# Performance work log

Hardware: AMD Instinct MI355X
Metric: run time of the kernel (lower is better)

Reference implementation:

```python
import jax, jax.numpy as jnp
import numpy as np

D_MODEL = 1024
N_HEADS = 16
D_HEAD = 64


def setup_inputs() -> dict:
    key = jax.random.key(0)
    ks = jax.random.split(key, 9)
    B, T = 2, 2048
    s_in = 1.0 / np.sqrt(D_MODEL)
    s_o = 1.0 / np.sqrt(N_HEADS * D_HEAD)
    return {
        "x": jax.random.normal(ks[0], (B, T, D_MODEL), dtype=jnp.float32),
        "wq": jax.random.normal(ks[1], (D_MODEL, N_HEADS * D_HEAD), dtype=jnp.float32) * s_in,
        "bq": jax.random.normal(ks[2], (N_HEADS * D_HEAD,), dtype=jnp.float32) * 0.01,
        "wk": jax.random.normal(ks[3], (D_MODEL, N_HEADS * D_HEAD), dtype=jnp.float32) * s_in,
        "bk": jax.random.normal(ks[4], (N_HEADS * D_HEAD,), dtype=jnp.float32) * 0.01,
        "wv": jax.random.normal(ks[5], (D_MODEL, N_HEADS * D_HEAD), dtype=jnp.float32) * s_in,
        "bv": jax.random.normal(ks[6], (N_HEADS * D_HEAD,), dtype=jnp.float32) * 0.01,
        "wo": jax.random.normal(ks[7], (N_HEADS * D_HEAD, D_MODEL), dtype=jnp.float32) * s_o,
        "bo": jax.random.normal(ks[8], (D_MODEL,), dtype=jnp.float32) * 0.01,
    }


def reference(x, wq, bq, wk, bk, wv, bv, wo, bo):
    B, T, _ = x.shape
    H, Dh = N_HEADS, D_HEAD
    # projections -> [B, H, T, Dh]
    q = (x @ wq + bq).reshape(B, T, H, Dh).transpose(0, 2, 1, 3)
    k = (x @ wk + bk).reshape(B, T, H, Dh).transpose(0, 2, 1, 3)
    v = (x @ wv + bv).reshape(B, T, H, Dh).transpose(0, 2, 1, 3)
    scale = 1.0 / np.sqrt(Dh).astype(np.float32)
    attn = jnp.einsum("bhqd,bhkd->bhqk", q, k) * scale  # [B,H,T,T]
    causal = jnp.tril(jnp.ones((T, T), dtype=bool))
    attn = jnp.where(causal, attn, jnp.float32(-jnp.inf))
    attn = jax.nn.softmax(attn, axis=-1)
    out = jnp.einsum("bhqk,bhkd->bhqd", attn, v)  # [B,H,T,Dh]
    out = out.transpose(0, 2, 1, 3).reshape(B, T, H * Dh)
    return out @ wo + bo
```

## Files before the change

kernel.cpp:

```cpp
#include <hip/hip_runtime.h>
#include <math.h>

#define D_MODEL 1024
#define N_HEADS 16
#define D_HEAD  64
#define B_SZ    2
#define T_SEQ   2048

typedef short bf16x8 __attribute__((ext_vector_type(8)));
typedef short bf16x4 __attribute__((ext_vector_type(4)));
typedef float f32x4  __attribute__((ext_vector_type(4)));
typedef unsigned short us4 __attribute__((ext_vector_type(4)));

__device__ __forceinline__ unsigned short f2bf(float f) {
  union { float f; unsigned u; } v; v.f = f;
  unsigned r = v.u + 0x7FFFu + ((v.u >> 16) & 1u);
  return (unsigned short)(r >> 16);
}
__device__ __forceinline__ float bf2f(unsigned short s) {
  union { unsigned u; float f; } v; v.u = ((unsigned)s) << 16;
  return v.f;
}
__device__ __forceinline__ unsigned pack2_rtz(float lo, float hi) {
  union { float f; unsigned u; } a, b; a.f = hi; b.f = lo;
  return __builtin_amdgcn_perm(a.u, b.u, 0x07060302u);
}

__device__ __forceinline__ void async_copy16(const unsigned short* g, unsigned short* l) {
  __builtin_amdgcn_global_load_lds(
      (__attribute__((address_space(1))) void*)(g),
      (__attribute__((address_space(3))) void*)(l), 16, 0, 0);
}

__global__ __launch_bounds__(256) void conv_all(
    const float* __restrict__ x,
    const float* __restrict__ wq, const float* __restrict__ wk,
    const float* __restrict__ wv, const float* __restrict__ wo,
    unsigned short* __restrict__ wt, unsigned short* __restrict__ xb)
{
  const int z = blockIdx.z;
  if (z < 4) {
    const float* W = (z == 0) ? wq : (z == 1) ? wk : (z == 2) ? wv : wo;
    unsigned short* O = wt + (size_t)z * D_MODEL * D_MODEL;
    __shared__ float t[32][33];
    const int tx = threadIdx.x & 31, ty = threadIdx.x >> 5;
    const int kb = blockIdx.x * 32, nb = blockIdx.y * 32;
    #pragma unroll
    for (int i = 0; i < 4; i++)
      t[ty + i * 8][tx] = W[(size_t)(kb + ty + i * 8) * D_MODEL + nb + tx];
    __syncthreads();
    #pragma unroll
    for (int i = 0; i < 4; i++)
      O[(size_t)(nb + ty + i * 8) * D_MODEL + kb + tx] = f2bf(t[tx][ty + i * 8]);
  } else {
    const int row = (z - 4) * 1024 + blockIdx.y * 32 + (threadIdx.x >> 3);
    const int col = blockIdx.x * 32 + (threadIdx.x & 7) * 4;
    float4 v = *(const float4*)&x[(size_t)row * D_MODEL + col];
    us4 o = { f2bf(v.x), f2bf(v.y), f2bf(v.z), f2bf(v.w) };
    *(us4*)&xb[(size_t)row * D_MODEL + col] = o;
  }
}

#define BKg 64
#define QSCALE 0.180336879f

__global__ __launch_bounds__(256) void qkv_gemm(
    const unsigned short* __restrict__ A, const unsigned short* __restrict__ Bt,
    const float* __restrict__ bq, const float* __restrict__ bk,
    const float* __restrict__ bv, unsigned short* __restrict__ qkv,
    unsigned short* __restrict__ vT)
{
  __shared__ unsigned short As[128 * BKg];
  __shared__ unsigned short Bs[64 * BKg];

  const int tid  = threadIdx.x;
  const int wv   = tid >> 6;
  const int lane = tid & 63;
  const int lr   = lane & 15;
  const int quad = lane >> 4;
  const int wm   = wv >> 1;
  const int wn   = wv & 1;
  const int row0 = blockIdx.x * 128;
  const int col0 = blockIdx.y * 64;
  const int K = D_MODEL;

  const int mid = col0 >> 10;
  const float* bias = (mid == 0) ? bq : (mid == 1) ? bk : bv;

  f32x4 acc[8];
  #pragma unroll
  for (int i = 0; i < 8; i++) acc[i] = (f32x4){0.f, 0.f, 0.f, 0.f};

  for (int k0 = 0; k0 < K; k0 += BKg) {
    #pragma unroll
    for (int it = 0; it < 4; it++) {
      const int gg = wv * 256 + it * 64 + lane;
      const int r  = gg >> 3;
      const int gc = ((gg & 7) ^ (r & 7)) * 8;
      async_copy16(A + (size_t)(row0 + r) * K + k0 + gc,
                   (unsigned short*)As + (size_t)(wv * 256 + it * 64) * 8);
    }
    #pragma unroll
    for (int it = 0; it < 2; it++) {
      const int gg = wv * 128 + it * 64 + lane;
      const int r  = gg >> 3;
      const int gc = ((gg & 7) ^ (r & 7)) * 8;
      async_copy16(Bt + (size_t)(col0 + r) * K + k0 + gc,
                   (unsigned short*)Bs + (size_t)(wv * 128 + it * 64) * 8);
    }
    __syncthreads();

    if (mid == 2) {
      bf16x8 aF[4][2], bF[2][2];
      #pragma unroll
      for (int hf = 0; hf < 2; hf++) {
        const int kc = (hf * 4 + quad) ^ (lr & 7);
        #pragma unroll
        for (int mi = 0; mi < 4; mi++)
          aF[mi][hf] = *(const bf16x8*)&As[(wm * 64 + mi * 16 + lr) * BKg + kc * 8];
        #pragma unroll
        for (int ni = 0; ni < 2; ni++)
          bF[ni][hf] = *(const bf16x8*)&Bs[(wn * 32 + ni * 16 + lr) * BKg + kc * 8];
      }
      #pragma unroll
      for (int hf = 0; hf < 2; hf++)
        #pragma unroll
        for (int mi = 0; mi < 4; mi++)
          #pragma unroll
          for (int ni = 0; ni < 2; ni++)
            acc[mi * 2 + ni] = __builtin_amdgcn_mfma_f32_16x16x32_bf16(
                aF[mi][hf], bF[ni][hf], acc[mi * 2 + ni], 0, 0, 0);
    } else {
      bf16x8 aF[2][2], bF[4][2];
      #pragma unroll
      for (int hf = 0; hf < 2; hf++) {
        const int kc = (hf * 4 + quad) ^ (lr & 7);
        #pragma unroll
        for (int mi = 0; mi < 2; mi++)
          aF[mi][hf] = *(const bf16x8*)&Bs[(wm * 32 + mi * 16 + lr) * BKg + kc * 8];
        #pragma unroll
        for (int ni = 0; ni < 4; ni++)
          bF[ni][hf] = *(const bf16x8*)&As[(wn * 64 + ni * 16 + lr) * BKg + kc * 8];
      }
      #pragma unroll
      for (int hf = 0; hf < 2; hf++)
        #pragma unroll
        for (int mi = 0; mi < 2; mi++)
          #pragma unroll
          for (int ni = 0; ni < 4; ni++)
            acc[mi * 4 + ni] = __builtin_amdgcn_mfma_f32_16x16x32_bf16(
                aF[mi][hf], bF[ni][hf], acc[mi * 4 + ni], 0, 0, 0);
    }
    __syncthreads();
  }

  if (mid == 2) {
    #pragma unroll
    for (int ni = 0; ni < 2; ni++) {
      const int nn = (col0 & 1023) + wn * 32 + ni * 16 + lr;
      const float bv_ = bias[nn];
      const int h = nn >> 6, d = nn & 63;
      #pragma unroll
      for (int mi = 0; mi < 4; mi++) {
        const int t0_ = row0 + wm * 64 + mi * 16 + quad * 4;
        const int b = t0_ >> 11, tl = t0_ & 2047;
        us4 o;
        #pragma unroll
        for (int i = 0; i < 4; i++) o[i] = f2bf(acc[mi * 2 + ni][i] + bv_);
        *(us4*)&vT[((size_t)(b * N_HEADS + h) * D_HEAD + d) * T_SEQ + tl] = o;
      }
    }
  } else {
    unsigned short* dst = qkv + (size_t)mid * (4096u * 1024u);
    const float qs = (mid == 0) ? QSCALE : 1.0f;
    #pragma unroll
    for (int ni = 0; ni < 4; ni++) {
      const int t = row0 + wn * 64 + ni * 16 + lr;
      const int b = t >> 11, tl = t & 2047;
      #pragma unroll
      for (int mi = 0; mi < 2; mi++) {
        const int f = (col0 & 1023) + wm * 32 + mi * 16 + quad * 4;
        const int h = f >> 6, d = f & 63;
        const float4 b4 = *(const float4*)&bias[f];
        us4 o;
        o[0] = f2bf((acc[mi * 4 + ni][0] + b4.x) * qs);
        o[1] = f2bf((acc[mi * 4 + ni][1] + b4.y) * qs);
        o[2] = f2bf((acc[mi * 4 + ni][2] + b4.z) * qs);
        o[3] = f2bf((acc[mi * 4 + ni][3] + b4.w) * qs);
        *(us4*)&dst[((size_t)(b * N_HEADS + h) * T_SEQ + tl) * D_HEAD + d] = o;
      }
    }
  }
}

__global__ __launch_bounds__(256) void mfma_gemm(
    const unsigned short* __restrict__ A, const unsigned short* __restrict__ Bt,
    const float* __restrict__ bias, float* __restrict__ C,
    int M, int N, int K)
{
  __shared__ unsigned short As[128 * BKg];
  __shared__ unsigned short Bs[64 * BKg];

  const int tid  = threadIdx.x;
  const int wv   = tid >> 6;
  const int lane = tid & 63;
  const int lr   = lane & 15;
  const int quad = lane >> 4;
  const int wm   = wv >> 1;
  const int wn   = wv & 1;
  const int row0 = blockIdx.x * 128;
  const int col0 = blockIdx.y * 64;

  f32x4 acc[4][2];
  #pragma unroll
  for (int mi = 0; mi < 4; mi++)
    #pragma unroll
    for (int ni = 0; ni < 2; ni++) acc[mi][ni] = (f32x4){0.f, 0.f, 0.f, 0.f};

  for (int k0 = 0; k0 < K; k0 += BKg) {
    #pragma unroll
    for (int it = 0; it < 4; it++) {
      const int gg = wv * 256 + it * 64 + lane;
      const int r  = gg >> 3;
      const int gc = ((gg & 7) ^ (r & 7)) * 8;
      async_copy16(A + (size_t)(row0 + r) * K + k0 + gc,
                   (unsigned short*)As + (size_t)(wv * 256 + it * 64) * 8);
    }
    #pragma unroll
    for (int it = 0; it < 2; it++) {
      const int gg = wv * 128 + it * 64 + lane;
      const int r  = gg >> 3;
      const int gc = ((gg & 7) ^ (r & 7)) * 8;
      async_copy16(Bt + (size_t)(col0 + r) * K + k0 + gc,
                   (unsigned short*)Bs + (size_t)(wv * 128 + it * 64) * 8);
    }
    __syncthreads();

    bf16x8 aF[4][2], bF[2][2];
    #pragma unroll
    for (int hf = 0; hf < 2; hf++) {
      const int kc = (hf * 4 + quad) ^ (lr & 7);
      #pragma unroll
      for (int mi = 0; mi < 4; mi++)
        aF[mi][hf] = *(const bf16x8*)&As[(wm * 64 + mi * 16 + lr) * BKg + kc * 8];
      #pragma unroll
      for (int ni = 0; ni < 2; ni++)
        bF[ni][hf] = *(const bf16x8*)&Bs[(wn * 32 + ni * 16 + lr) * BKg + kc * 8];
    }
    #pragma unroll
    for (int hf = 0; hf < 2; hf++)
      #pragma unroll
      for (int mi = 0; mi < 4; mi++)
        #pragma unroll
        for (int ni = 0; ni < 2; ni++)
          acc[mi][ni] = __builtin_amdgcn_mfma_f32_16x16x32_bf16(
              aF[mi][hf], bF[ni][hf], acc[mi][ni], 0, 0, 0);
    __syncthreads();
  }

  #pragma unroll
  for (int ni = 0; ni < 2; ni++) {
    const int n = col0 + wn * 32 + ni * 16 + lr;
    const float bv = bias[n];
    #pragma unroll
    for (int mi = 0; mi < 4; mi++) {
      #pragma unroll
      for (int i = 0; i < 4; i++) {
        const int m = row0 + wm * 64 + mi * 16 + quad * 4 + i;
        C[(size_t)m * N + n] = acc[mi][ni][i] + bv;
      }
    }
  }
}

__global__ __launch_bounds__(256) void flash_part(
    const unsigned short* __restrict__ Q, const unsigned short* __restrict__ K,
    const unsigned short* __restrict__ Vt, unsigned short* __restrict__ Out,
    unsigned short* __restrict__ Opart, float* __restrict__ Lpart)
{
  const int bh = blockIdx.x;
  const int y  = blockIdx.y;
  int g, md;
  if (y < 20) {
    const int k = y / 5, r = y % 5;
    if (r == 0) { g = 7 - k; md = 0; }
    else        { g = 15 - 2 * k - ((r - 1) >> 1); md = 1 + ((r - 1) & 1); }
  } else { g = 3 - (y - 20); md = 0; }

  const int b  = bh >> 4;
  const int h  = bh & 15;

  const unsigned short* Qb = Q  + (size_t)bh * T_SEQ * D_HEAD;
  const unsigned short* Kb = K  + (size_t)bh * T_SEQ * D_HEAD;
  const unsigned short* Vb = Vt + (size_t)bh * D_HEAD * T_SEQ;

  __shared__ __align__(16) unsigned short Ks[2][64 * 64];
  __shared__ __align__(16) unsigned short Vs[2][64 * 64];

  const int tid  = threadIdx.x;
  const int wv4  = tid >> 6;
  const int lane = tid & 63;
  const int lr   = lane & 15;
  const int quad = lane >> 4;

  const int qg      = 4 * g + wv4;
  const int q0      = qg * 32;
  const int my_full = 2 * g + 1 + (wv4 >> 1);
  const int tstart  = (md == 2) ? (g + 1) : 0;
  const int bend    = (md == 1) ? (g + 1) : (2 * g + 2);
  const int my_end  = (md == 1) ? (g + 1) : my_full;

  const int cbase = (tid & ~63);
  auto stage = [&](int buf, int tile) {
    const unsigned short* ksrc = Kb + (size_t)tile * 64 * D_HEAD;
    const int kv0 = tile * 64;
    #pragma unroll
    for (int it = 0; it < 2; it++) {
      const int gg = it * 256 + tid;
      const int r  = gg >> 3;
      const int gc = (gg & 7) ^ (r & 7);
      async_copy16(ksrc + r * 64 + gc * 8, &Ks[buf][(size_t)(it * 256 + cbase) * 8]);
      async_copy16(Vb + (size_t)r * T_SEQ + kv0 + gc * 8, &Vs[buf][(size_t)(it * 256 + cbase) * 8]);
    }
  };

  bf16x8 bQ[2][2];
  #pragma unroll
  for (int qb = 0; qb < 2; qb++)
    #pragma unroll
    for (int kh = 0; kh < 2; kh++)
      bQ[qb][kh] = *(const bf16x8*)&Qb[(size_t)(q0 + qb * 16 + lr) * D_HEAD + kh * 32 + quad * 8];

  f32x4 oacc[2][4];
  #pragma unroll
  for (int qb = 0; qb < 2; qb++)
    #pragma unroll
    for (int dt = 0; dt < 4; dt++) oacc[qb][dt] = (f32x4){0.f, 0.f, 0.f, 0.f};
  f32x4 lacc[2] = {(f32x4){0.f, 0.f, 0.f, 0.f}, (f32x4){0.f, 0.f, 0.f, 0.f}};

  const bf16x4 vONE = {(short)0x3F80, (short)0x3F80, (short)0x3F80, (short)0x3F80};

  int cur = 0;
  stage(0, tstart);

  for (int j = tstart; j < bend; j++) {
    __syncthreads();
    const bool act = (j < my_end);
    const unsigned short* KsB = &Ks[cur][0];
    const unsigned short* VsB = &Vs[cur][0];
    const int kv0 = j * 64;

    bf16x8 aK[4][2];
    bf16x4 aV[4][4];
    if (act) {
      #pragma unroll
      for (int nt = 0; nt < 4; nt++) {
        const int row = nt * 16 + lr;
        #pragma unroll
        for (int kh = 0; kh < 2; kh++) {
          const int sc = (kh * 4 + quad) ^ (row & 7);
          aK[nt][kh] = *(const bf16x8*)&KsB[row * 64 + sc * 8];
        }
      }
      #pragma unroll
      for (int dt = 0; dt < 4; dt++) {
        const int row = dt * 16 + lr;
        #pragma unroll
        for (int ks = 0; ks < 4; ks++) {
          const int sc = (ks * 2 + (quad >> 1)) ^ (row & 7);
          aV[dt][ks] = *(const bf16x4*)&VsB[row * 64 + sc * 8 + (quad & 1) * 4];
        }
      }
    }

    if (j + 1 < bend) stage(cur ^ 1, j + 1);

    if (act) {
      f32x4 sacc[2][4];
      __builtin_amdgcn_s_setprio(1);
      #pragma unroll
      for (int nt = 0; nt < 4; nt++) {
        #pragma unroll
        for (int qb = 0; qb < 2; qb++) {
          f32x4 c = (f32x4){0.f, 0.f, 0.f, 0.f};
          c = __builtin_amdgcn_mfma_f32_16x16x32_bf16(aK[nt][0], bQ[qb][0], c, 0, 0, 0);
          c = __builtin_amdgcn_mfma_f32_16x16x32_bf16(aK[nt][1], bQ[qb][1], c, 0, 0, 0);
          sacc[qb][nt] = c;
        }
      }
      __builtin_amdgcn_s_setprio(0);

      const bool diag = (j == my_full - 1);
      bf16x4 bP[2][4];
      #pragma unroll
      for (int qb = 0; qb < 2; qb++) {
        if (diag) {
          const int qcol = q0 + qb * 16 + lr;
          #pragma unroll
          for (int nt = 0; nt < 4; nt++)
            #pragma unroll
            for (int i = 0; i < 4; i++)
              if (kv0 + nt * 16 + quad * 4 + i > qcol) sacc[qb][nt][i] = -INFINITY;
        }
        #pragma unroll
        for (int nt = 0; nt < 4; nt++) {
          float p[4];
          #pragma unroll
          for (int i = 0; i < 4; i++)
            p[i] = __builtin_amdgcn_exp2f(sacc[qb][nt][i]);
          union { unsigned u[2]; bf16x4 v; } pk;
          pk.u[0] = pack2_rtz(p[0], p[1]);
          pk.u[1] = pack2_rtz(p[2], p[3]);
          bP[qb][nt] = pk.v;
        }
      }

      __builtin_amdgcn_s_setprio(1);
      #pragma unroll
      for (int ks = 0; ks < 4; ks++) {
        #pragma unroll
        for (int qb = 0; qb < 2; qb++) {
          lacc[qb] = __builtin_amdgcn_mfma_f32_16x16x16bf16_1k(
              vONE, bP[qb][ks], lacc[qb], 0, 0, 0);
          #pragma unroll
          for (int dt = 0; dt < 4; dt++)
            oacc[qb][dt] = __builtin_amdgcn_mfma_f32_16x16x16bf16_1k(
                aV[dt][ks], bP[qb][ks], oacc[qb][dt], 0, 0, 0);
        }
      }
      __builtin_amdgcn_s_setprio(0);
    }
    cur ^= 1;
  }

  float l_i[2] = {lacc[0][0], lacc[1][0]};

  if (md == 0) {
    #pragma unroll
    for (int qb = 0; qb < 2; qb++) {
      const float invl = __builtin_amdgcn_rcpf(l_i[qb]);
      const size_t orow = (size_t)(b * T_SEQ + q0 + qb * 16 + lr) * D_MODEL + h * D_HEAD;
      #pragma unroll
      for (int dt = 0; dt < 4; dt++) {
        us4 o;
        #pragma unroll
        for (int i = 0; i < 4; i++) o[i] = f2bf(oacc[qb][dt][i] * invl);
        *(us4*)&Out[orow + dt * 16 + quad * 4] = o;
      }
    }
  } else {
    const int s = md - 1;
    const int p = (bh * 32 + (qg - 32)) * 2 + s;
    #pragma unroll
    for (int qb = 0; qb < 2; qb++) {
      Lpart[(p * 2 + qb) * 64 + lane] = l_i[qb];
      #pragma unroll
      for (int dt = 0; dt < 4; dt++) {
        us4 o;
        #pragma unroll
        for (int i = 0; i < 4; i++) o[i] = f2bf(oacc[qb][dt][i]);
        *(us4*)&Opart[(size_t)(((p * 8 + qb * 4 + dt) * 64) + lane) * 4] = o;
      }
    }
  }
}

__global__ __launch_bounds__(64) void flash_reduce(
    const unsigned short* __restrict__ Opart, const float* __restrict__ Lpart,
    unsigned short* __restrict__ Out)
{
  const int bh  = blockIdx.x;
  const int qgr = blockIdx.y;
  const int q0  = (32 + qgr) * 32;
  const int b   = bh >> 4;
  const int h   = bh & 15;
  const int lane = threadIdx.x;
  const int lr   = lane & 15;
  const int quad = lane >> 4;

  const int item = bh * 32 + qgr;
  const int p0 = item * 2, p1 = item * 2 + 1;

  #pragma unroll
  for (int qb = 0; qb < 2; qb++) {
    const float l0 = Lpart[(p0 * 2 + qb) * 64 + lane];
    const float l1 = Lpart[(p1 * 2 + qb) * 64 + lane];
    const float invL = __builtin_amdgcn_rcpf(l0 + l1);
    const size_t orow = (size_t)(b * T_SEQ + q0 + qb * 16 + lr) * D_MODEL + h * D_HEAD;
    #pragma unroll
    for (int dt = 0; dt < 4; dt++) {
      us4 o0 = *(const us4*)&Opart[(size_t)(((p0 * 8 + qb * 4 + dt) * 64) + lane) * 4];
      us4 o1 = *(const us4*)&Opart[(size_t)(((p1 * 8 + qb * 4 + dt) * 64) + lane) * 4];
      us4 o;
      #pragma unroll
      for (int i = 0; i < 4; i++)
        o[i] = f2bf((bf2f(o0[i]) + bf2f(o1[i])) * invL);
      *(us4*)&Out[orow + dt * 16 + quad * 4] = o;
    }
  }
}

extern "C" void kernel_launch(void* const* d_in, const int* in_sizes, int n_in,
                              void* d_out, int out_size, void* d_ws, size_t ws_size,
                              hipStream_t stream) {
  (void)in_sizes; (void)n_in; (void)out_size; (void)ws_size;

  const float* x  = (const float*)d_in[0];
  const float* wq = (const float*)d_in[1];
  const float* bq = (const float*)d_in[2];
  const float* wk = (const float*)d_in[3];
  const float* bk = (const float*)d_in[4];
  const float* wv = (const float*)d_in[5];
  const float* bv = (const float*)d_in[6];
  const float* wo = (const float*)d_in[7];
  const float* bo = (const float*)d_in[8];
  float* out = (float*)d_out;

  const int M = B_SZ * T_SEQ;
  const int N = D_MODEL;
  const int K = D_MODEL;
  const size_t MN = (size_t)M * N;
  const size_t WN = (size_t)N * N;

  unsigned short* wt    = (unsigned short*)d_ws;
  unsigned short* xb    = wt + 4 * WN;
  unsigned short* qkv   = xb + MN;
  unsigned short* qb    = qkv;
  unsigned short* kb    = qkv + MN;
  unsigned short* vT    = qkv + 2 * MN;
  unsigned short* attnb = vT + MN;
  float* Lpart = (float*)(attnb + MN);
  unsigned short* Opart = xb;

  conv_all<<<dim3(32, 32, 8), dim3(256), 0, stream>>>(x, wq, wk, wv, wo, wt, xb);

  qkv_gemm<<<dim3(M / 128, 48), dim3(256), 0, stream>>>(xb, wt, bq, bk, bv, qkv, vT);

  flash_part<<<dim3(B_SZ * N_HEADS, 24), dim3(256), 0, stream>>>(
      qb, kb, vT, attnb, Opart, Lpart);
  flash_reduce<<<dim3(B_SZ * N_HEADS, 32), dim3(64), 0, stream>>>(
      Opart, Lpart, attnb);

  mfma_gemm<<<dim3(M / 128, N / 64), dim3(256), 0, stream>>>(attnb, wt + 3 * WN, bo, out, M, N, K);
}
```

Measured before the change: 188.3 us.

## Split more causal query groups across two KV halves for finer load balance

The flash attention work split changes from 24 to 30 blocks per head. Query groups 2 through 15 are now each split into two KV-range halves, and only groups 0 and 1 run unsplit, which gives more, smaller work items so the CUs are better balanced. The partial outputs outgrow the old scratch area, so they spill across the now-dead wq/wk/wv weight region and the xb buffer, and the reduce kernel grows to 56 items per head. Two smaller changes ride along: the stage loop precomputes swizzled K/V base pointers, and Lpart stores only 16 values per qb instead of 64 redundant ones. The cost is more partial-output traffic and reduce work, plus a dependence on the weight scratch being dead after qkv_gemm.

```diff
diff --git a/kernel.cpp b/kernel.cpp
--- a/kernel.cpp
+++ b/kernel.cpp
@@ -30,6 +30,13 @@
   __builtin_amdgcn_global_load_lds(
       (__attribute__((address_space(1))) void*)(g),
       (__attribute__((address_space(3))) void*)(l), 16, 0, 0);
+}
+
+__device__ __forceinline__ unsigned short* opart_ptr(
+    unsigned short* wtd, unsigned short* xbd, int p) {
+  const size_t off = (size_t)p * 2048;
+  const size_t RA  = (size_t)3 * 1024 * 1024;
+  return (off < RA) ? (wtd + off) : (xbd + (off - RA));
 }
 
 __global__ __launch_bounds__(256) void conv_all(
@@ -276,16 +283,14 @@
 __global__ __launch_bounds__(256) void flash_part(
     const unsigned short* __restrict__ Q, const unsigned short* __restrict__ K,
     const unsigned short* __restrict__ Vt, unsigned short* __restrict__ Out,
-    unsigned short* __restrict__ Opart, float* __restrict__ Lpart)
+    unsigned short* __restrict__ OpA, unsigned short* __restrict__ OpB,
+    float* __restrict__ Lpart)
 {
   const int bh = blockIdx.x;
   const int y  = blockIdx.y;
   int g, md;
-  if (y < 20) {
-    const int k = y / 5, r = y % 5;
-    if (r == 0) { g = 7 - k; md = 0; }
-    else        { g = 15 - 2 * k - ((r - 1) >> 1); md = 1 + ((r - 1) & 1); }
-  } else { g = 3 - (y - 20); md = 0; }
+  if (y < 28) { g = 15 - (y >> 1); md = 1 + (y & 1); }
+  else        { g = 29 - y; md = 0; }
 
   const int b  = bh >> 4;
   const int h  = bh & 15;
@@ -311,17 +316,18 @@
   const int my_end  = (md == 1) ? (g + 1) : my_full;
 
   const int cbase = (tid & ~63);
+  const int rr = tid >> 3;
+  const int gcf = ((tid & 7) ^ (rr & 7)) * 8;
+  const unsigned short* kp0 = Kb + (size_t)rr * D_HEAD + gcf;
+  const unsigned short* vp0 = Vb + (size_t)rr * T_SEQ + gcf;
+
   auto stage = [&](int buf, int tile) {
-    const unsigned short* ksrc = Kb + (size_t)tile * 64 * D_HEAD;
-    const int kv0 = tile * 64;
-    #pragma unroll
-    for (int it = 0; it < 2; it++) {
-      const int gg = it * 256 + tid;
-      const int r  = gg >> 3;
-      const int gc = (gg & 7) ^ (r & 7);
-      async_copy16(ksrc + r * 64 + gc * 8, &Ks[buf][(size_t)(it * 256 + cbase) * 8]);
-      async_copy16(Vb + (size_t)r * T_SEQ + kv0 + gc * 8, &Vs[buf][(size_t)(it * 256 + cbase) * 8]);
-    }
+    const unsigned short* kt = kp0 + (size_t)tile * (64 * D_HEAD);
+    const unsigned short* vt = vp0 + (size_t)tile * 64;
+    async_copy16(kt,                    &Ks[buf][(size_t)cbase * 8]);
+    async_copy16(kt + 32 * D_HEAD,      &Ks[buf][(size_t)(256 + cbase) * 8]);
+    async_copy16(vt,                    &Vs[buf][(size_t)cbase * 8]);
+    async_copy16(vt + (size_t)32 * T_SEQ, &Vs[buf][(size_t)(256 + cbase) * 8]);
   };
 
   bf16x8 bQ[2][2];
@@ -450,47 +456,53 @@
     }
   } else {
     const int s = md - 1;
-    const int p = (bh * 32 + (qg - 32)) * 2 + s;
+    const int p = (bh * 56 + (qg - 8)) * 2 + s;
+    unsigned short* Op = opart_ptr(OpA, OpB, p);
+    if (quad == 0) {
+      Lpart[(p * 2 + 0) * 16 + lr] = l_i[0];
+      Lpart[(p * 2 + 1) * 16 + lr] = l_i[1];
+    }
     #pragma unroll
     for (int qb = 0; qb < 2; qb++) {
-      Lpart[(p * 2 + qb) * 64 + lane] = l_i[qb];
       #pragma unroll
       for (int dt = 0; dt < 4; dt++) {
         us4 o;
         #pragma unroll
         for (int i = 0; i < 4; i++) o[i] = f2bf(oacc[qb][dt][i]);
-        *(us4*)&Opart[(size_t)(((p * 8 + qb * 4 + dt) * 64) + lane) * 4] = o;
+        *(us4*)&Op[(size_t)(((qb * 4 + dt) * 64) + lane) * 4] = o;
       }
     }
   }
 }
 
 __global__ __launch_bounds__(64) void flash_reduce(
-    const unsigned short* __restrict__ Opart, const float* __restrict__ Lpart,
-    unsigned short* __restrict__ Out)
+    unsigned short* __restrict__ OpA, unsigned short* __restrict__ OpB,
+    const float* __restrict__ Lpart, unsigned short* __restrict__ Out)
 {
   const int bh  = blockIdx.x;
   const int qgr = blockIdx.y;
-  const int q0  = (32 + qgr) * 32;
+  const int q0  = (8 + qgr) * 32;
   const int b   = bh >> 4;
   const int h   = bh & 15;
   const int lane = threadIdx.x;
   const int lr   = lane & 15;
   const int quad = lane >> 4;
 
-  const int item = bh * 32 + qgr;
+  const int item = bh * 56 + qgr;
   const int p0 = item * 2, p1 = item * 2 + 1;
+  const unsigned short* O0 = opart_ptr(OpA, OpB, p0);
+  const unsigned short* O1 = opart_ptr(OpA, OpB, p1);
 
   #pragma unroll
   for (int qb = 0; qb < 2; qb++) {
-    const float l0 = Lpart[(p0 * 2 + qb) * 64 + lane];
-    const float l1 = Lpart[(p1 * 2 + qb) * 64 + lane];
+    const float l0 = Lpart[(p0 * 2 + qb) * 16 + lr];
+    const float l1 = Lpart[(p1 * 2 + qb) * 16 + lr];
     const float invL = __builtin_amdgcn_rcpf(l0 + l1);
     const size_t orow = (size_t)(b * T_SEQ + q0 + qb * 16 + lr) * D_MODEL + h * D_HEAD;
     #pragma unroll
     for (int dt = 0; dt < 4; dt++) {
-      us4 o0 = *(const us4*)&Opart[(size_t)(((p0 * 8 + qb * 4 + dt) * 64) + lane) * 4];
-      us4 o1 = *(const us4*)&Opart[(size_t)(((p1 * 8 + qb * 4 + dt) * 64) + lane) * 4];
+      us4 o0 = *(const us4*)&O0[(size_t)(((qb * 4 + dt) * 64) + lane) * 4];
+      us4 o1 = *(const us4*)&O1[(size_t)(((qb * 4 + dt) * 64) + lane) * 4];
       us4 o;
       #pragma unroll
       for (int i = 0; i < 4; i++)
@@ -530,16 +542,15 @@
   unsigned short* vT    = qkv + 2 * MN;
   unsigned short* attnb = vT + MN;
   float* Lpart = (float*)(attnb + MN);
-  unsigned short* Opart = xb;
 
   conv_all<<<dim3(32, 32, 8), dim3(256), 0, stream>>>(x, wq, wk, wv, wo, wt, xb);
 
   qkv_gemm<<<dim3(M / 128, 48), dim3(256), 0, stream>>>(xb, wt, bq, bk, bv, qkv, vT);
 
-  flash_part<<<dim3(B_SZ * N_HEADS, 24), dim3(256), 0, stream>>>(
-      qb, kb, vT, attnb, Opart, Lpart);
-  flash_reduce<<<dim3(B_SZ * N_HEADS, 32), dim3(64), 0, stream>>>(
-      Opart, Lpart, attnb);
+  flash_part<<<dim3(B_SZ * N_HEADS, 30), dim3(256), 0, stream>>>(
+      qb, kb, vT, attnb, wt, xb, Lpart);
+  flash_reduce<<<dim3(B_SZ * N_HEADS, 56), dim3(64), 0, stream>>>(
+      wt, xb, Lpart, attnb);
 
   mfma_gemm<<<dim3(M / 128, N / 64), dim3(256), 0, stream>>>(attnb, wt + 3 * WN, bo, out, M, N, K);
 }
```

Result: no change. 185.1 us (-1.7%).
